# Optimization experiments

Hardware: AMD Instinct MI355X
Metric: run time of the kernel (lower is better)

Reference implementation:

```python
import jax, jax.numpy as jnp
import numpy as np

# ---- static configuration (matches init_kwargs) ----
B = 8; CIN = 3; COUT = 3
H_IN, W_IN = 128, 256          # img_size
H, W = 32, 64                  # internal grid = img_size / scale_factor
E = 256; HID = 512             # embed_dim, mlp hidden (ratio 2)
NR, NPHI = 3, 4                # DISCO kernel_shape
K = 1 + (NR - 1) * NPHI        # 9 piecewise-linear basis functions
LMAX = MMAX = H                # SHT truncation on internal grid
PI = np.pi

# ---- DISCO basis: psi[k, ho, hi, dlon] (quadrature folded in), stored as conj(rfft) over lon ----
def _build_psi(nlat_in, nlon_in, nlat_out, cutoff):
    ti = PI * (np.arange(nlat_in) + 0.5) / nlat_in
    to = PI * (np.arange(nlat_out) + 0.5) / nlat_out
    ph = 2 * PI * np.arange(nlon_in) / nlon_in
    cto, sto = np.cos(to)[:, None, None], np.sin(to)[:, None, None]
    cti, sti = np.cos(ti)[None, :, None], np.sin(ti)[None, :, None]
    cph, sph = np.cos(ph)[None, None, :], np.sin(ph)[None, None, :]
    r = np.arccos(np.clip(cto * cti + sto * sti * cph, -1.0, 1.0))      # great-circle dist
    alpha = np.arctan2(sti * sph, cti * sto - sti * cto * cph)          # azimuth
    dr = cutoff / (NR - 1); dphi = 2 * PI / NPHI
    quad = (sti * (PI / nlat_in) * (2 * PI / nlon_in)) * (r <= cutoff)  # quadrature * cutoff mask
    psi = np.empty((K, nlat_out, nlat_in, nlon_in), np.float32)
    psi[0] = np.clip(1 - r / dr, 0, 1) * quad                           # isotropic center basis
    for j in range(1, NR):
        tr = np.clip(1 - np.abs(r - j * dr) / dr, 0, 1)
        for k in range(NPHI):
            d = np.abs(np.mod(alpha - k * dphi + PI, 2 * PI) - PI)
            psi[1 + (j - 1) * NPHI + k] = tr * np.clip(1 - d / dphi, 0, 1) * quad
    return np.conj(np.fft.rfft(psi, axis=-1)).astype(np.complex64)

PSIH_ENC = jnp.asarray(_build_psi(H_IN, W_IN, H, 4 * PI / (H - 1)))
PSIH_INT = jnp.asarray(_build_psi(H, W, H, 4 * (NR + 1) * PI / (H - 1)))
PSIH_DEC = jnp.asarray(_build_psi(H_IN, W_IN, H_IN, 4 * PI / (H - 1)))

# ---- normalized associated Legendre for SHT on internal equiangular grid ----
def _legendre(lmax, theta):
    ct, st = np.cos(theta), np.sin(theta)
    P = np.zeros((lmax, lmax, theta.size))
    P[0, 0] = 1.0 / np.sqrt(2.0)
    for m in range(1, lmax):
        P[m, m] = np.sqrt((2 * m + 1) / (2.0 * m)) * st * P[m - 1, m - 1]
    for m in range(lmax - 1):
        P[m + 1, m] = np.sqrt(2 * m + 3.0) * ct * P[m, m]
    for m in range(lmax):
        for l in range(m + 2, lmax):
            a = np.sqrt((4.0 * l * l - 1) / (l * l - m * m))
            b = a * np.sqrt(((l - 1.0) ** 2 - m * m) / (4.0 * (l - 1) ** 2 - 1))
            P[l, m] = a * ct * P[l - 1, m] - b * P[l - 2, m]
    return P  # [l, m, h]

_THETA = PI * (np.arange(H) + 0.5) / H
_P = _legendre(LMAX, _THETA).astype(np.float32)
PW = jnp.asarray(_P * (np.sin(_THETA) * (PI / H))[None, None, :])  # analysis (with quadrature)
PT = jnp.asarray(_P)                                                # synthesis

# ---- bilinear resample (32,64)->(128,256), periodic in lon ----
_fi = np.clip((np.arange(H_IN) + 0.5) * H / H_IN - 0.5, 0, H - 1)
LAT_I0 = jnp.asarray(np.floor(_fi).astype(np.int32))
LAT_I1 = jnp.asarray(np.minimum(np.floor(_fi).astype(np.int32) + 1, H - 1))
LAT_W = jnp.asarray((_fi - np.floor(_fi)).astype(np.float32))
_fj = np.arange(W_IN) * W / W_IN
LON_J0 = jnp.asarray((np.floor(_fj).astype(np.int32)) % W)
LON_J1 = jnp.asarray((np.floor(_fj).astype(np.int32) + 1) % W)
LON_W = jnp.asarray((_fj - np.floor(_fj)).astype(np.float32))


def _disco(x, psih, n_in, stride):
    # circular cross-correlation over lon via FFT: z[b,c,k,ho,wo]
    Xh = jnp.fft.rfft(x, axis=-1)
    Zh = jnp.einsum('khim,bcim->bckhm', psih, Xh)
    return jnp.fft.irfft(Zh, n=n_in, axis=-1)[..., ::stride]


def _spectral(x, w):
    # driscoll-healy spectral conv: per-l channel mixing in SH space
    Xh = jnp.fft.rfft(x, axis=-1)[..., :MMAX]
    c = jnp.einsum('lmh,bchm->bclm', PW, Xh)
    c = jnp.einsum('ocl,bclm->bolm', w, c)
    Xo = jnp.einsum('lmh,bolm->bohm', PT, c)
    Xo = jnp.pad(Xo, ((0, 0), (0, 0), (0, 0), (0, W // 2 + 1 - MMAX)))
    return jnp.fft.irfft(Xo, n=W, axis=-1)


def _resample(x):
    a = jnp.take(x, LAT_I0, axis=2) * (1 - LAT_W)[:, None] + jnp.take(x, LAT_I1, axis=2) * LAT_W[:, None]
    return jnp.take(a, LON_J0, axis=3) * (1 - LON_W) + jnp.take(a, LON_J1, axis=3) * LON_W


def _forward(x, enc_w, lconv_w, gconv_w, mlp_w1, mlp_b1, mlp_w2, mlp_b2, skip_w, skip_b, dec_w):
    # encoder: DISCO conv (128,256)->(32,64), CIN->E
    z = _disco(x, PSIH_ENC, W_IN, W_IN // W)          # [B,CIN,K,32,64]
    x = jnp.einsum('ock,bckhw->bohw', enc_w, z)       # [B,E,32,64]
    for i in range(4):
        res = x
        if i % 2 == 0:  # local DISCO block
            z = _disco(x, PSIH_INT, W, 1)
            x = jnp.einsum('ock,bckhw->bohw', lconv_w[i // 2], z)
        else:           # global spectral (SHT) block
            x = _spectral(x, gconv_w[i // 2])
        # MLP (1x1 convs) + linear outer skip (norm = Identity)
        h = jax.nn.relu(jnp.einsum('oc,bchw->bohw', mlp_w1[i], x) + mlp_b1[i][:, None, None])
        x = jnp.einsum('oc,bchw->bohw', mlp_w2[i], h) + mlp_b2[i][:, None, None]
        x = x + jnp.einsum('oc,bchw->bohw', skip_w[i], res) + skip_b[i][:, None, None]
    # decoder: bilinear upsample then DISCO conv at full res, E->COUT (mix channels first: COUT small)
    x = _resample(x)                                  # [B,E,128,256]
    u = jnp.einsum('ock,bchw->bokhw', dec_w, x)       # [B,COUT,K,128,256]
    Uh = jnp.fft.rfft(u, axis=-1)
    Yh = jnp.einsum('khim,bokim->bohm', PSIH_DEC, Uh)
    return jnp.fft.irfft(Yh, n=W_IN, axis=-1)         # [B,COUT,128,256]


def setup_inputs() -> dict:
    key = jax.random.key(0)
    ks = jax.random.split(key, 8)
    f = jnp.float32
    return dict(
        x=jax.random.normal(ks[0], (B, CIN, H_IN, W_IN), f),
        enc_w=jax.random.normal(ks[1], (E, CIN, K), f) * float(1 / np.sqrt(CIN * K)),
        lconv_w=jax.random.normal(ks[2], (2, E, E, K), f) * float(1 / np.sqrt(E * K)),
        gconv_w=jax.random.normal(ks[3], (2, E, E, LMAX), f) * float(1 / np.sqrt(E)),
        mlp_w1=jax.random.normal(ks[4], (4, HID, E), f) * float(np.sqrt(2.0 / E)),
        mlp_b1=jnp.zeros((4, HID), f),
        mlp_w2=jax.random.normal(ks[5], (4, E, HID), f) * float(1 / np.sqrt(HID)),
        mlp_b2=jnp.zeros((4, E), f),
        skip_w=jax.random.normal(ks[6], (4, E, E), f) * float(np.sqrt(0.5 / E)),
        skip_b=jnp.zeros((4, E), f),
        dec_w=jax.random.normal(ks[7], (COUT, E, K), f) * float(1 / np.sqrt(E * K)),
    )


def reference(x, enc_w, lconv_w, gconv_w, mlp_w1, mlp_b1, mlp_w2, mlp_b2, skip_w, skip_b, dec_w):
    return _forward(x, enc_w, lconv_w, gconv_w, mlp_w1, mlp_b1, mlp_w2, mlp_b2, skip_w, skip_b, dec_w)
```

## Files before the change

kernel.cpp:

```cpp
#include <hip/hip_runtime.h>
#include <math.h>
#include <utility>

#define DI __device__ __forceinline__

namespace {

typedef unsigned short u16;
typedef unsigned int u32;
using f16x8 = __attribute__((ext_vector_type(8))) _Float16;
using f32x4 = __attribute__((ext_vector_type(4))) float;

constexpr int BB  = 8;
constexpr int CIN = 3;
constexpr int HIN = 128, WIN = 256;
constexpr int EE  = 256;
constexpr int NSP = BB * 32 * 64;
constexpr double PI_D = 3.14159265358979323846;
constexpr int ME_ENC = 5120, ME_INT = 2048, ME_DEC = 4608;
constexpr int HW_E = 34;

DI u16 f16rne(float x) { _Float16 h = (_Float16)x; return __builtin_bit_cast(unsigned short, h); }
DI float f16tof(u16 u) { return (float)__builtin_bit_cast(_Float16, u); }
DI u32 packhl(float v) {
  u16 h = f16rne(v);
  u16 l = f16rne(v - f16tof(h));
  return (u32)h | ((u32)l << 16);
}

DI bool psi_point(int nlat_in, int nlon_in, int nlat_out, double cutoff,
                  int ho, int hi, int d, bool wantv, float* out9)
{
  double ti = PI_D * (hi + 0.5) / nlat_in;
  double to = PI_D * (ho + 0.5) / nlat_out;
  double ph = 2.0 * PI_D * d / nlon_in;
  double cto = cos(to), sto = sin(to);
  double cti = cos(ti), sti = sin(ti);
  double cph = cos(ph), sph = sin(ph);
  double ca = cto * cti + sto * sti * cph;
  ca = fmin(1.0, fmax(-1.0, ca));
  double r = acos(ca);
  if (r > cutoff) return false;
  if (wantv) {
    double dr   = cutoff * 0.5;
    double dphi = PI_D * 0.5;
    double quad = sti * (PI_D / nlat_in) * (2.0 * PI_D / nlon_in);
    out9[0] = (float)(fmin(1.0, fmax(0.0, 1.0 - r / dr)) * quad);
    double alpha = atan2(sti * sph, cti * sto - sti * cto * cph);
#pragma unroll
    for (int j = 1; j <= 2; ++j) {
      double tr = fmin(1.0, fmax(0.0, 1.0 - fabs(r - j * dr) / dr));
#pragma unroll
      for (int k2 = 0; k2 < 4; ++k2) {
        double xx = alpha - k2 * dphi + PI_D;
        double yy = xx - 2.0 * PI_D * floor(xx / (2.0 * PI_D));
        double dd = fabs(yy - PI_D);
        out9[1 + (j - 1) * 4 + k2] = (float)(tr * fmin(1.0, fmax(0.0, 1.0 - dd / dphi)) * quad);
      }
    }
  }
  return true;
}

__global__ void k_psi_count(int nlat_in, int nlon_in, int nlat_out, double cutoff, int* cnt)
{
  int hi = blockIdx.x, ho = blockIdx.y, d = threadIdx.x;
  float dummy[9];
  bool in = psi_point(nlat_in, nlon_in, nlat_out, cutoff, ho, hi, d, false, dummy);
  unsigned long long mask = __ballot(in);
  if ((threadIdx.x & 63) == 0) {
    int tot = __popcll(mask);
    if (tot) atomicAdd(cnt + ho * nlat_in + hi, tot);
  }
}

__global__ void k_psi_scan(int nlat_in, int maxe, int* cnt, int* offs)
{
  int ho = blockIdx.x;
  int* c = cnt + ho * nlat_in;
  int* o = offs + ho * (nlat_in + 1);
  int run = 0;
  for (int hi = 0; hi < nlat_in; ++hi) {
    o[hi] = run < maxe ? run : maxe;
    run += c[hi];
    c[hi] = 0;
  }
  o[nlat_in] = run < maxe ? run : maxe;
}

__global__ void k_psi_fill(int nlat_in, int nlon_in, int nlat_out, double cutoff,
                           int maxe, int* cnt, const int* __restrict__ offs, float* __restrict__ tab)
{
  int hi = blockIdx.x, ho = blockIdx.y, d = threadIdx.x;
  float p9[9];
  bool in = psi_point(nlat_in, nlon_in, nlat_out, cutoff, ho, hi, d, true, p9);
  unsigned long long mask = __ballot(in);
  int lane = threadIdx.x & 63;
  int tot = __popcll(mask);
  int wbase = 0;
  if (lane == 0 && tot) wbase = atomicAdd(cnt + ho * nlat_in + hi, tot);
  wbase = __shfl(wbase, 0, 64);
  if (in) {
    int rank = __popcll(mask & ((1ull << lane) - 1ull));
    int idx = offs[ho * (nlat_in + 1) + hi] + wbase + rank;
    if (idx < maxe) {
      float* te = tab + ((size_t)ho * maxe + idx) * 12;
      te[0] = __int_as_float((hi << 16) | d);
#pragma unroll
      for (int k = 0; k < 9; ++k) te[1 + k] = p9[k];
      te[10] = 0.f; te[11] = 0.f;
    }
  }
}

__global__ void k_legendre(float* __restrict__ PW, float* __restrict__ PT)
{
  int h = threadIdx.x;
  if (h >= 32) return;
  double th = PI_D * (h + 0.5) / 32.0;
  double ct = cos(th), st = sin(th);
  double quad = st * (PI_D / 32.0);
  double diag = 0.70710678118654752440;
  for (int m = 0; m < 32; ++m) {
    if (m > 0) diag = sqrt((2.0 * m + 1.0) / (2.0 * m)) * st * diag;
    double plm2 = diag;
    PT[((size_t)m * 32 + m) * 32 + h] = (float)plm2;
    PW[((size_t)m * 32 + m) * 32 + h] = (float)(plm2 * quad);
    if (m + 1 < 32) {
      double plm1 = sqrt(2.0 * m + 3.0) * ct * diag;
      PT[((size_t)(m + 1) * 32 + m) * 32 + h] = (float)plm1;
      PW[((size_t)(m + 1) * 32 + m) * 32 + h] = (float)(plm1 * quad);
      for (int l = m + 2; l < 32; ++l) {
        double a  = sqrt((4.0 * l * l - 1.0) / ((double)l * l - (double)m * m));
        double bb = a * sqrt((((double)(l - 1) * (l - 1)) - (double)m * m) /
                             (4.0 * (double)(l - 1) * (l - 1) - 1.0));
        double p = a * ct * plm1 - bb * plm2;
        PT[((size_t)l * 32 + m) * 32 + h] = (float)p;
        PW[((size_t)l * 32 + m) * 32 + h] = (float)(p * quad);
        plm2 = plm1; plm1 = p;
      }
    }
    for (int l = 0; l < m; ++l) {
      PT[((size_t)l * 32 + m) * 32 + h] = 0.f;
      PW[((size_t)l * 32 + m) * 32 + h] = 0.f;
    }
  }
}

__global__ void k_tw(float* tc, float* ts)
{
  int t = blockIdx.x * 256 + threadIdx.x;
  if (t >= 33 * 64) return;
  int m = t >> 6, w = t & 63;
  double th = 2.0 * PI_D * m * w / 64.0;
  tc[t] = (float)cos(th);
  ts[t] = (float)sin(th);
}

__global__ void k_tw2(float* tc256, float* ts256, float* tc64, float* ts64)
{
  int t = threadIdx.x;
  double th = 2.0 * PI_D * t / 256.0;
  tc256[t] = (float)cos(th);
  ts256[t] = (float)sin(th);
  if (t < 64) {
    double th2 = 2.0 * PI_D * t / 64.0;
    tc64[t] = (float)cos(th2);
    ts64[t] = (float)sin(th2);
  }
}

__global__ void k_twmat(u32* __restrict__ tw256, u32* __restrict__ itw256,
                        u32* __restrict__ tw64, u32* __restrict__ itw64,
                        u32* __restrict__ iffold)
{
  int t = blockIdx.x * 256 + threadIdx.x;
  if (t < 256 * 129) {
    int w = t / 129, m = t % 129;
    double th = 2.0 * PI_D * ((m * w) & 255) / 256.0;
    tw256[w * 258 + 2 * m]     = packhl((float)cos(th));
    tw256[w * 258 + 2 * m + 1] = packhl((float)(-sin(th)));
  }
  if (t < 129 * 256) {
    int m = t >> 8, w = t & 255;
    double th = 2.0 * PI_D * ((m * w) & 255) / 256.0;
    float cr, ci;
    if (m == 0)        { cr = 1.f / 256.f; ci = 0.f; }
    else if (m == 128) { cr = ((w & 1) ? -1.f : 1.f) / 256.f; ci = 0.f; }
    else { cr = (float)(2.0 * cos(th) / 256.0); ci = (float)(-2.0 * sin(th) / 256.0); }
    itw256[(2 * m) * 256 + w] = packhl(cr);
    if (2 * m + 1 < 258) itw256[(2 * m + 1) * 256 + w] = packhl(ci);
  }
  if (t < 64 * 33) {
    int w = t / 33, m = t % 33;
    double th = 2.0 * PI_D * ((m * w) & 63) / 64.0;
    tw64[w * 66 + 2 * m]     = packhl((float)cos(th));
    tw64[w * 66 + 2 * m + 1] = packhl((float)(-sin(th)));
  }
  if (t < 33 * 64) {
    int m = t >> 6, w = t & 63;
    double th = 2.0 * PI_D * ((m * w) & 63) / 64.0;
    float cr, ci;
    if (m == 0)       { cr = 1.f / 64.f; ci = 0.f; }
    else if (m == 32) { cr = ((w & 1) ? -1.f : 1.f) / 64.f; ci = 0.f; }
    else { cr = (float)(2.0 * cos(th) / 64.0); ci = (float)(-2.0 * sin(th) / 64.0); }
    itw64[(2 * m) * 64 + w] = packhl(cr);
    if (2 * m + 1 < 66) itw64[(2 * m + 1) * 64 + w] = packhl(ci);
  }
  if (t < 129 * 64) {
    int m = t >> 6, wo = t & 63;
    double th = 2.0 * PI_D * ((m * wo) & 63) / 64.0;
    float cr, ci;
    if (m == 0)        { cr = 1.f / 256.f; ci = 0.f; }
    else if (m == 128) { cr = 1.f / 256.f; ci = 0.f; }
    else { cr = (float)(2.0 * cos(th) / 256.0); ci = (float)(-2.0 * sin(th) / 256.0); }
    iffold[(2 * m) * 64 + wo] = packhl(cr);
    if (2 * m + 1 < 258) iffold[(2 * m + 1) * 64 + wo] = packhl(ci);
  }
}

__global__ __launch_bounds__(256) void k_split(const float* __restrict__ in,
                                               u32* __restrict__ out, int n)
{
  for (int i = blockIdx.x * 256 + threadIdx.x; i < n; i += gridDim.x * 256)
    out[i] = packhl(in[i]);
}

__global__ void k_gwT_lp(const float* __restrict__ gw, u32* __restrict__ gwTlp)
{
  int idx = blockIdx.x * 256 + threadIdx.x;
  int c = idx & 255, o = (idx >> 8) & 255, l = idx >> 16;
  gwTlp[idx] = packhl(gw[((size_t)o * 256 + c) * 32 + l]);
}

__global__ void k_decT(const float* __restrict__ dw, float* __restrict__ dt)
{
  int idx = blockIdx.x * 256 + threadIdx.x;
  if (idx >= 27 * 256) return;
  int c = idx & 255, ok = idx >> 8;
  int o = ok / 9, k = ok % 9;
  dt[idx] = dw[((size_t)o * 256 + c) * 9 + k];
}

__global__ __launch_bounds__(320) void k_psih_dec(const int* __restrict__ off,
    const float* __restrict__ tab, const float* __restrict__ tc, const float* __restrict__ ts,
    float* __restrict__ psih)
{
  int ho = blockIdx.x, hw = blockIdx.y;
  int hi = ho - 16 + hw;
  int t = threadIdx.x;
  if (t >= 258) return;
  int m = t >> 1, ri = t & 1;
  const float* tw = ri ? ts : tc;
  float acc[9] = {};
  if (hi >= 0 && hi < 128) {
    int e0 = off[ho * 129 + hi], e1 = off[ho * 129 + hi + 1];
    const float* tb = tab + ((size_t)ho * ME_DEC + e0) * 12;
    for (int e = e0; e < e1; ++e, tb += 12) {
      int d = __float_as_int(tb[0]) & 0xffff;
      float v = tw[(m * d) & 255];
#pragma unroll
      for (int k = 0; k < 9; ++k) acc[k] += tb[1 + k] * v;
    }
  }
  size_t base = ((size_t)(ho * 33 + hw) * 9) * 258 + 2 * m + ri;
#pragma unroll
  for (int k = 0; k < 9; ++k) psih[base + (size_t)k * 258] = acc[k];
}

__global__ __launch_bounds__(128) void k_psih_int(const int* __restrict__ off,
    const float* __restrict__ tab, const float* __restrict__ tc, const float* __restrict__ ts,
    float* __restrict__ psih)
{
  int ho = blockIdx.x, hi = blockIdx.y;
  int t = threadIdx.x;
  if (t >= 66) return;
  int m = t >> 1, ri = t & 1;
  const float* tw = ri ? ts : tc;
  float acc[9] = {};
  int e0 = off[ho * 33 + hi], e1 = off[ho * 33 + hi + 1];
  const float* tb = tab + ((size_t)ho * ME_INT + e0) * 12;
  for (int e = e0; e < e1; ++e, tb += 12) {
    int d = __float_as_int(tb[0]) & 0xffff;
    float v = tw[(m * d) & 63];
#pragma unroll
    for (int k = 0; k < 9; ++k) acc[k] += tb[1 + k] * v;
  }
  size_t base = ((size_t)(ho * 32 + hi) * 9) * 66 + 2 * m + ri;
#pragma unroll
  for (int k = 0; k < 9; ++k) psih[base + (size_t)k * 66] = acc[k];
}

__global__ __launch_bounds__(320) void k_psih_enc(const int* __restrict__ off,
    const float* __restrict__ tab, const float* __restrict__ tc, const float* __restrict__ ts,
    float* __restrict__ psih)
{
  int ho = blockIdx.x, hw = blockIdx.y;
  int hi = 4 * ho - 15 + hw;
  int t = threadIdx.x;
  if (t >= 258) return;
  int m = t >> 1, ri = t & 1;
  const float* tw = ri ? ts : tc;
  float acc[9] = {};
  if (hi >= 0 && hi < 128) {
    int e0 = off[ho * 129 + hi], e1 = off[ho * 129 + hi + 1];
    const float* tb = tab + ((size_t)ho * ME_ENC + e0) * 12;
    for (int e = e0; e < e1; ++e, tb += 12) {
      int d = __float_as_int(tb[0]) & 0xffff;
      float v = tw[(m * d) & 255];
#pragma unroll
      for (int k = 0; k < 9; ++k) acc[k] += tb[1 + k] * v;
    }
  }
  size_t base = ((size_t)(ho * HW_E + hw) * 9) * 258 + 2 * m + ri;
#pragma unroll
  for (int k = 0; k < 9; ++k) psih[base + (size_t)k * 258] = acc[k];
}

__global__ __launch_bounds__(192) void k_enc_mconv(const float* __restrict__ psih,
    const float* __restrict__ XhE, float* __restrict__ Zh)
{
  int ho = blockIdx.x, cb = blockIdx.y;
  int c = cb >> 3, b = cb & 7;
  int m = threadIdx.x;
  if (m > 128) return;
  const float2* X2 = (const float2*)XhE;
  const float2* P2 = (const float2*)psih;
  float zr[9] = {}, zi[9] = {};
  int hi0 = 4 * ho - 15;
  for (int hw = 0; hw < HW_E; ++hw) {
    int hi = hi0 + hw;
    if (hi < 0 || hi > 127) continue;
    float2 xv = X2[((size_t)(b * 3 + c) * 128 + hi) * 129 + m];
    size_t pb = ((size_t)(ho * HW_E + hw) * 9) * 129 + m;
#pragma unroll
    for (int k = 0; k < 9; ++k) {
      float2 p = P2[pb + (size_t)k * 129];
      zr[k] += p.x * xv.x - p.y * xv.y;
      zi[k] += p.x * xv.y + p.y * xv.x;
    }
  }
#pragma unroll
  for (int k = 0; k < 9; ++k)
    ((float2*)Zh)[(((size_t)(c * 9 + k) * 8 + b) * 32 + ho) * 129 + m] =
        make_float2(zr[k], zi[k]);
}

__global__ __launch_bounds__(320) void k_int_mconv(const float* __restrict__ xh,
    const float* __restrict__ psih, float* __restrict__ zh, int c0)
{
  int ho = blockIdx.x, g = blockIdx.y, b = blockIdx.z;
  int t = threadIdx.x;
  if (t >= 264) return;
  int cl = t / 33, m = t % 33;
  int c = c0 + g * 8 + cl;
  const float2* X2 = (const float2*)xh;
  const float2* P2 = (const float2*)psih;
  float zr[9] = {}, zi[9] = {};
  for (int hi = 0; hi < 32; ++hi) {
    float2 xv = X2[((size_t)(c * 8 + b) * 32 + hi) * 33 + m];
    size_t pb = ((size_t)(ho * 32 + hi) * 9) * 33 + m;
#pragma unroll
    for (int k = 0; k < 9; ++k) {
      float2 p = P2[pb + (size_t)k * 33];
      zr[k] += p.x * xv.x - p.y * xv.y;
      zi[k] += p.x * xv.y + p.y * xv.x;
    }
  }
  int crow = (g * 8 + cl) * 9;
#pragma unroll
  for (int k = 0; k < 9; ++k)
    ((float2*)zh)[((size_t)(crow + k)) * 8448 + b * 1056 + ho * 33 + m] =
        make_float2(zr[k], zi[k]);
}

__global__ __launch_bounds__(192) void k_dec_mconv(const float* __restrict__ psih,
    const float* __restrict__ gh, float* __restrict__ yh)
{
  int ho = blockIdx.x, b = blockIdx.y;
  int m = threadIdx.x;
  if (m > 128) return;
  const float2* P2 = (const float2*)psih;
  const float2* G2 = (const float2*)gh;
  float yr[3] = {}, yi[3] = {};
  for (int hw = 0; hw < 33; ++hw) {
    int hi = ho - 16 + hw;
    if (hi < 0 || hi > 127) continue;
    size_t pb = ((size_t)(ho * 33 + hw) * 9) * 129 + m;
#pragma unroll
    for (int k = 0; k < 9; ++k) {
      float2 p = P2[pb + (size_t)k * 129];
#pragma unroll
      for (int o = 0; o < 3; ++o) {
        float2 gv = G2[((size_t)((o * 9 + k) * 8 + b) * 128 + hi) * 129 + m];
        yr[o] += p.x * gv.x - p.y * gv.y;
        yi[o] += p.x * gv.y + p.y * gv.x;
      }
    }
  }
#pragma unroll
  for (int o = 0; o < 3; ++o)
    ((float2*)yh)[((size_t)(b * 3 + o) * 128 + ho) * 129 + m] = make_float2(yr[o], yi[o]);
}

__global__ __launch_bounds__(256) void k_gemm(
    int M, int N, int K,
    const float* __restrict__ A, const u32* __restrict__ Ap, int lda, long long sA,
    const float* __restrict__ Bm, const u32* __restrict__ Bp, int ldb, long long sB,
    float* __restrict__ C, int ldc, long long sC,
    const float* __restrict__ bias, int flags)
{
  if (A)  A  += (size_t)blockIdx.z * sA;
  if (Ap) Ap += (size_t)blockIdx.z * sA;
  if (Bm) Bm += (size_t)blockIdx.z * sB;
  if (Bp) Bp += (size_t)blockIdx.z * sB;
  C += (size_t)blockIdx.z * sC;
  __shared__ alignas(16) u16 Ah[128 * 40], Al[128 * 40], Bh[128 * 40], Bl[128 * 40];
  int bm = blockIdx.y * 128, bn = blockIdx.x * 128;
  int tid = threadIdx.x;
  int sr = tid >> 1, k2 = tid & 1;
  int lane = tid & 63, wid = tid >> 6;
  int wr = wid >> 1, wc = wid & 1;
  int lrow = lane & 15, kg = lane >> 4;
  f32x4 acc[4][4] = {};
  bool bok = (bn + sr) < N;

  for (int k0 = 0; k0 < K; k0 += 32) {
    {
      u32* ph = (u32*)&Ah[sr * 40 + k2 * 16];
      u32* pl = (u32*)&Al[sr * 40 + k2 * 16];
      if (Ap) {
        const u32* Ar = Ap + (size_t)(bm + sr) * lda + k0 + k2 * 16;
#pragma unroll
        for (int j2 = 0; j2 < 8; ++j2) {
          int gk = k0 + k2 * 16 + 2 * j2;
          u32 w0 = (gk < K)     ? Ar[2 * j2]     : 0u;
          u32 w1 = (gk + 1 < K) ? Ar[2 * j2 + 1] : 0u;
          ph[j2] = (w0 & 0xffffu) | (w1 << 16);
          pl[j2] = (w0 >> 16) | (w1 & 0xffff0000u);
        }
      } else {
        const float* Ar = A + (size_t)(bm + sr) * lda + k0 + k2 * 16;
#pragma unroll
        for (int j2 = 0; j2 < 8; ++j2) {
          int gk = k0 + k2 * 16 + 2 * j2;
          float v0 = (gk < K)     ? Ar[2 * j2]     : 0.f;
          float v1 = (gk + 1 < K) ? Ar[2 * j2 + 1] : 0.f;
          u16 h0 = f16rne(v0), h1 = f16rne(v1);
          u16 l0 = f16rne(v0 - f16tof(h0)), l1 = f16rne(v1 - f16tof(h1));
          ph[j2] = (u32)h0 | ((u32)h1 << 16);
          pl[j2] = (u32)l0 | ((u32)l1 << 16);
        }
      }
    }
    {
      u32* ph = (u32*)&Bh[sr * 40 + k2 * 16];
      u32* pl = (u32*)&Bl[sr * 40 + k2 * 16];
      if (Bp) {
        const u32* Bc = Bp + bn + sr;
#pragma unroll
        for (int j2 = 0; j2 < 8; ++j2) {
          int gk = k0 + k2 * 16 + 2 * j2;
          u32 w0 = (bok && gk < K)     ? Bc[(size_t)gk * ldb]       : 0u;
          u32 w1 = (bok && gk + 1 < K) ? Bc[(size_t)(gk + 1) * ldb] : 0u;
          ph[j2] = (w0 & 0xffffu) | (w1 << 16);
          pl[j2] = (w0 >> 16) | (w1 & 0xffff0000u);
        }
      } else {
        const float* Bc = Bm + bn + sr;
#pragma unroll
        for (int j2 = 0; j2 < 8; ++j2) {
          int gk = k0 + k2 * 16 + 2 * j2;
          float v0 = (bok && gk < K)     ? Bc[(size_t)gk * ldb]       : 0.f;
          float v1 = (bok && gk + 1 < K) ? Bc[(size_t)(gk + 1) * ldb] : 0.f;
          u16 h0 = f16rne(v0), h1 = f16rne(v1);
          u16 l0 = f16rne(v0 - f16tof(h0)), l1 = f16rne(v1 - f16tof(h1));
          ph[j2] = (u32)h0 | ((u32)h1 << 16);
          pl[j2] = (u32)l0 | ((u32)l1 << 16);
        }
      }
    }
    __syncthreads();
    f16x8 fah[4], fal[4], fbh[4], fbl[4];
#pragma unroll
    for (int i = 0; i < 4; ++i) {
      int ar = wr * 64 + i * 16 + lrow;
      fah[i] = *(const f16x8*)&Ah[ar * 40 + kg * 8];
      fal[i] = *(const f16x8*)&Al[ar * 40 + kg * 8];
      int br = wc * 64 + i * 16 + lrow;
      fbh[i] = *(const f16x8*)&Bh[br * 40 + kg * 8];
      fbl[i] = *(const f16x8*)&Bl[br * 40 + kg * 8];
    }
#pragma unroll
    for (int i = 0; i < 4; ++i)
#pragma unroll
      for (int j = 0; j < 4; ++j) {
        acc[i][j] = __builtin_amdgcn_mfma_f32_16x16x32_f16(fah[i], fbh[j], acc[i][j], 0, 0, 0);
        acc[i][j] = __builtin_amdgcn_mfma_f32_16x16x32_f16(fah[i], fbl[j], acc[i][j], 0, 0, 0);
        acc[i][j] = __builtin_amdgcn_mfma_f32_16x16x32_f16(fal[i], fbh[j], acc[i][j], 0, 0, 0);
      }
    __syncthreads();
  }

#pragma unroll
  for (int i = 0; i < 4; ++i) {
    int gm0 = bm + wr * 64 + i * 16 + kg * 4;
#pragma unroll
    for (int j = 0; j < 4; ++j) {
      int gn = bn + wc * 64 + j * 16 + lrow;
      if (gn >= N) continue;
#pragma unroll
      for (int rr = 0; rr < 4; ++rr) {
        int gm = gm0 + rr;
        size_t idx = (size_t)gm * ldc + gn;
        float v = acc[i][j][rr];
        if (flags & 4) v += bias[gm];
        if (flags & 2) v += C[idx];
        if (flags & 1) v = fmaxf(v, 0.f);
        C[idx] = v;
      }
    }
  }
}

__global__ __launch_bounds__(256) void k_gemm_m27(const float* __restrict__ A,
    const float* __restrict__ Bm, float* __restrict__ C)
{
  int n = blockIdx.x * 256 + threadIdx.x;
  float acc[27] = {};
  for (int k = 0; k < 256; ++k) {
    float bv = Bm[(size_t)k * NSP + n];
#pragma unroll
    for (int m = 0; m < 27; ++m) acc[m] += A[m * 256 + k] * bv;
  }
#pragma unroll
  for (int m = 0; m < 27; ++m) C[(size_t)m * NSP + n] = acc[m];
}

__global__ __launch_bounds__(64) void k_analysis(const float* __restrict__ PW,
    const float* __restrict__ Xh, float* __restrict__ c1)
{
  int l = blockIdx.x, c = blockIdx.y, b = blockIdx.z;
  int t = threadIdx.x, m = t >> 1, ri = t & 1;
  const float* xr = Xh + ((size_t)(c * 8 + b) * 32) * 66;
  const float* pw = PW + ((size_t)l * 32 + m) * 32;
  float acc = 0.f;
  for (int h = 0; h < 32; ++h) acc += pw[h] * xr[h * 66 + 2 * m + ri];
  c1[(((size_t)l * EE + c) * 8 + b) * 64 + 2 * m + ri] = acc;
}

__global__ __launch_bounds__(64) void k_synth(const float* __restrict__ PT,
    const float* __restrict__ c2, const float* __restrict__ tc, const float* __restrict__ ts,
    float* __restrict__ outact)
{
  int h = blockIdx.x, o = blockIdx.y, b = blockIdx.z;
  int t = threadIdx.x;
  __shared__ float Xo[64];
  {
    int m = t >> 1, ri = t & 1;
    float acc = 0.f;
    for (int l = m; l < 32; ++l)
      acc += PT[((size_t)l * 32 + m) * 32 + h] *
             c2[(((size_t)l * EE + o) * 8 + b) * 64 + 2 * m + ri];
    Xo[t] = acc;
  }
  __syncthreads();
  float y = Xo[0];
  for (int m = 1; m < 32; ++m)
    y += 2.f * (Xo[2 * m] * tc[m * 64 + t] - Xo[2 * m + 1] * ts[m * 64 + t]);
  outact[(size_t)o * NSP + b * 2048 + h * 64 + t] = y * (1.f / 64.f);
}

__global__ __launch_bounds__(256) void k_resample(const float* __restrict__ gi, float* __restrict__ gf)
{
  int t = blockIdx.x * 256 + threadIdx.x;
  int WO = t & 255, HO = (t >> 8) & 127, b = (t >> 15) & 7, ok = t >> 18;
  float fi = fminf(fmaxf(HO * 0.25f - 0.375f, 0.f), 31.f);
  int i0 = (int)fi;
  int i1 = min(i0 + 1, 31);
  float wi = fi - (float)i0;
  int j0 = WO >> 2;
  int j1 = (j0 + 1) & 63;
  float wj = (float)(WO & 3) * 0.25f;
  const float* s = gi + (size_t)ok * NSP + b * 2048;
  float v00 = s[i0 * 64 + j0], v01 = s[i0 * 64 + j1];
  float v10 = s[i1 * 64 + j0], v11 = s[i1 * 64 + j1];
  float a0 = v00 * (1.f - wj) + v01 * wj;
  float a1 = v10 * (1.f - wj) + v11 * wj;
  gf[((size_t)ok * 8 + b) * 32768 + HO * 256 + WO] = a0 * (1.f - wi) + a1 * wi;
}

}

extern "C" void kernel_launch(void* const* d_in, const int* in_sizes, int n_in,
                              void* d_out, int out_size, void* d_ws, size_t ws_size,
                              hipStream_t stream)
{
  const float* x_in  = (const float*)d_in[0];
  const float* enc_w = (const float*)d_in[1];
  const float* lconv = (const float*)d_in[2];
  const float* gconv = (const float*)d_in[3];
  const float* w1    = (const float*)d_in[4];
  const float* b1    = (const float*)d_in[5];
  const float* w2    = (const float*)d_in[6];
  const float* b2    = (const float*)d_in[7];
  const float* skw   = (const float*)d_in[8];
  const float* skb   = (const float*)d_in[9];
  const float* decw  = (const float*)d_in[10];
  float* out = (float*)d_out;

  char* ws = (char*)d_ws;
  size_t off = 0;
  auto alloc = [&](size_t nfloats) -> float* {
    float* p = (float*)(ws + off);
    off += ((nfloats * 4 + 255) / 256) * 256;
    return p;
  };
  float* PW    = alloc(32768);
  float* PT    = alloc(32768);
  float* tcos  = alloc(33 * 64);
  float* tsin  = alloc(33 * 64);
  float* tc256 = alloc(256);
  float* ts256 = alloc(256);
  float* tc64  = alloc(64);
  float* ts64  = alloc(64);
  u32* TW256p  = (u32*)alloc(256 * 258);
  u32* ITW256p = (u32*)alloc(258 * 256);
  u32* TW64p   = (u32*)alloc(64 * 66);
  u32* ITW64p  = (u32*)alloc(66 * 64);
  u32* IFp     = (u32*)alloc(258 * 64);
  int*   cnt2  = (int*)alloc(21504);
  int*   cnt_enc = cnt2;
  int*   cnt_int = cnt2 + 4096;
  int*   cnt_dec = cnt2 + 5120;
  int*   off_enc = (int*)alloc(32 * 129);
  int*   off_int = (int*)alloc(32 * 33);
  int*   off_dec = (int*)alloc(128 * 129);
  float* decT     = alloc(27 * 256);
  float* psih_dec = alloc((size_t)128 * 33 * 9 * 258);
  float* psih_int = alloc((size_t)32 * 32 * 9 * 66);
  float* psih_enc = alloc((size_t)32 * HW_E * 9 * 258);
  u32* enc_wp = (u32*)alloc(256 * 27);
  u32* w1p    = (u32*)alloc(4 * 512 * 256);
  u32* w2p    = (u32*)alloc(4 * 256 * 512);
  u32* skwp   = (u32*)alloc(4 * 256 * 256);
  u32* lconvp = (u32*)alloc(2 * 256 * 2304);
  float* P  = alloc((size_t)EE * NSP);
  float* Q  = alloc((size_t)EE * NSP);
  float* T  = alloc((size_t)EE * NSP);
  float* U  = alloc(18382848);
  (void)ws_size; (void)in_sizes; (void)n_in; (void)out_size;

  float* tab_dec = U;
  float* tab_int = U + 7077888;
  float* tab_enc = U + 7864320;
  float* zc      = U;
  float* XhE     = U + 442368;
  float* ZhE     = U + 1234944;
  float* XH      = U;
  float* ZH      = U + 4325376;
  float* XO      = U + 14057472;
  float* c1s     = U + 4325376;
  float* c2s     = U + 8519680;
  u32*   gwTlp   = (u32*)(U + 12713984);
  float* Hb      = U;
  u32*   DYNp    = (u32*)(U + 8388608);
  float* g_int   = U;
  float* g_full  = U + 524288;
  float* GH      = U + 7602176;
  float* YH      = U + 14735360;

  const double CUT_LOC = 4.0 * PI_D / 31.0;
  const double CUT_INT = 16.0 * PI_D / 31.0;
  auto splitN = [&](const float* src, u32* dst, int n) {
    int g = (n + 255) / 256; if (g > 2048) g = 2048;
    hipLaunchKernelGGL(k_split, dim3(g), dim3(256), 0, stream, src, dst, n);
  };

  hipMemsetAsync(cnt2, 0, 21504 * 4, stream);
  hipLaunchKernelGGL(k_legendre, dim3(1), dim3(64), 0, stream, PW, PT);
  hipLaunchKernelGGL(k_tw,  dim3(9), dim3(256), 0, stream, tcos, tsin);
  hipLaunchKernelGGL(k_tw2, dim3(1), dim3(256), 0, stream, tc256, ts256, tc64, ts64);
  hipLaunchKernelGGL(k_twmat, dim3(129), dim3(256), 0, stream, TW256p, ITW256p, TW64p, ITW64p, IFp);
  hipLaunchKernelGGL(k_decT, dim3(27), dim3(256), 0, stream, decw, decT);
  splitN(enc_w, enc_wp, 256 * 27);
  splitN(w1,    w1p,    4 * 512 * 256);
  splitN(w2,    w2p,    4 * 256 * 512);
  splitN(skw,   skwp,   4 * 256 * 256);
  splitN(lconv, lconvp, 2 * 256 * 2304);

  hipLaunchKernelGGL(k_psi_count, dim3(128, 32), dim3(256), 0, stream, 128, 256, 32, CUT_LOC, cnt_enc);
  hipLaunchKernelGGL(k_psi_scan,  dim3(32), dim3(1), 0, stream, 128, ME_ENC, cnt_enc, off_enc);
  hipLaunchKernelGGL(k_psi_fill,  dim3(128, 32), dim3(256), 0, stream, 128, 256, 32, CUT_LOC, ME_ENC, cnt_enc, off_enc, tab_enc);

  hipLaunchKernelGGL(k_psi_count, dim3(32, 32), dim3(64), 0, stream, 32, 64, 32, CUT_INT, cnt_int);
  hipLaunchKernelGGL(k_psi_scan,  dim3(32), dim3(1), 0, stream, 32, ME_INT, cnt_int, off_int);
  hipLaunchKernelGGL(k_psi_fill,  dim3(32, 32), dim3(64), 0, stream, 32, 64, 32, CUT_INT, ME_INT, cnt_int, off_int, tab_int);

  hipLaunchKernelGGL(k_psi_count, dim3(128, 128), dim3(256), 0, stream, 128, 256, 128, CUT_LOC, cnt_dec);
  hipLaunchKernelGGL(k_psi_scan,  dim3(128), dim3(1), 0, stream, 128, ME_DEC, cnt_dec, off_dec);
  hipLaunchKernelGGL(k_psi_fill,  dim3(128, 128), dim3(256), 0, stream, 128, 256, 128, CUT_LOC, ME_DEC, cnt_dec, off_dec, tab_dec);

  hipLaunchKernelGGL(k_psih_dec, dim3(128, 33), dim3(320), 0, stream, off_dec, tab_dec, tc256, ts256, psih_dec);
  hipLaunchKernelGGL(k_psih_int, dim3(32, 32),  dim3(128), 0, stream, off_int, tab_int, tc64, ts64, psih_int);
  hipLaunchKernelGGL(k_psih_enc, dim3(32, HW_E), dim3(320), 0, stream, off_enc, tab_enc, tc256, ts256, psih_enc);

  hipLaunchKernelGGL(k_gemm, dim3(3, 24, 1), dim3(256), 0, stream,
                     3072, 258, 256, x_in, (const u32*)nullptr, 256, 0LL,
                     (const float*)nullptr, TW256p, 258, 0LL,
                     XhE, 258, 0LL, (const float*)nullptr, 0);
  hipLaunchKernelGGL(k_enc_mconv, dim3(32, 24), dim3(192), 0, stream, psih_enc, XhE, ZhE);
  hipLaunchKernelGGL(k_gemm, dim3(1, 54, 1), dim3(256), 0, stream,
                     6912, 64, 258, ZhE, (const u32*)nullptr, 258, 0LL,
                     (const float*)nullptr, IFp, 64, 0LL,
                     zc, 64, 0LL, (const float*)nullptr, 0);
  hipLaunchKernelGGL(k_gemm, dim3(128, 2, 1), dim3(256), 0, stream,
                     256, NSP, 27, (const float*)nullptr, enc_wp, 27, 0LL,
                     zc, (const u32*)nullptr, NSP, 0LL,
                     P, NSP, 0LL, (const float*)nullptr, 0);

  for (int i = 0; i < 4; ++i) {
    int layer = i >> 1;
    if ((i & 1) == 0) {
      hipLaunchKernelGGL(k_gemm, dim3(1, 512, 1), dim3(256), 0, stream,
                         65536, 66, 64, P, (const u32*)nullptr, 64, 0LL,
                         (const float*)nullptr, TW64p, 66, 0LL,
                         XH, 66, 0LL, (const float*)nullptr, 0);
      for (int cc = 0; cc < 4; ++cc) {
        hipLaunchKernelGGL(k_int_mconv, dim3(32, 8, 8), dim3(320), 0, stream,
                           XH, psih_int, ZH, cc * 64);
        hipLaunchKernelGGL(k_gemm, dim3(132, 2, 1), dim3(256), 0, stream,
                           256, 16896, 576,
                           (const float*)nullptr, lconvp + (size_t)layer * 589824 + cc * 576, 2304, 0LL,
                           ZH, (const u32*)nullptr, 16896, 0LL,
                           XO, 16896, 0LL, (const float*)nullptr, cc ? 2 : 0);
      }
      hipLaunchKernelGGL(k_gemm, dim3(1, 512, 1), dim3(256), 0, stream,
                         65536, 64, 66, XO, (const u32*)nullptr, 66, 0LL,
                         (const float*)nullptr, ITW64p, 64, 0LL,
                         T, 64, 0LL, (const float*)nullptr, 0);
    } else {
      hipLaunchKernelGGL(k_gwT_lp, dim3(8192), dim3(256), 0, stream,
                         gconv + (size_t)layer * 2097152, gwTlp);
      hipLaunchKernelGGL(k_gemm, dim3(1, 512, 1), dim3(256), 0, stream,
                         65536, 66, 64, P, (const u32*)nullptr, 64, 0LL,
                         (const float*)nullptr, TW64p, 66, 0LL,
                         XH, 66, 0LL, (const float*)nullptr, 0);
      hipLaunchKernelGGL(k_analysis, dim3(32, 256, 8), dim3(64), 0, stream, PW, XH, c1s);
      hipLaunchKernelGGL(k_gemm, dim3(4, 2, 32), dim3(256), 0, stream,
                         256, 512, 256,
                         (const float*)nullptr, gwTlp, 256, 65536LL,
                         c1s, (const u32*)nullptr, 512, 131072LL,
                         c2s, 512, 131072LL, (const float*)nullptr, 0);
      hipLaunchKernelGGL(k_synth, dim3(32, 256, 8), dim3(64), 0, stream, PT, c2s, tcos, tsin, T);
    }
    splitN(T, DYNp, EE * NSP);
    hipLaunchKernelGGL(k_gemm, dim3(128, 4, 1), dim3(256), 0, stream,
                       512, NSP, 256, (const float*)nullptr, w1p + (size_t)i * 131072, 256, 0LL,
                       (const float*)nullptr, DYNp, NSP, 0LL,
                       Hb, NSP, 0LL, b1 + (size_t)i * 512, 5);
    splitN(Hb, DYNp, 512 * NSP);
    hipLaunchKernelGGL(k_gemm, dim3(128, 2, 1), dim3(256), 0, stream,
                       256, NSP, 512, (const float*)nullptr, w2p + (size_t)i * 131072, 512, 0LL,
                       (const float*)nullptr, DYNp, NSP, 0LL,
                       Q, NSP, 0LL, b2 + (size_t)i * 256, 4);
    splitN(P, DYNp, EE * NSP);
    hipLaunchKernelGGL(k_gemm, dim3(128, 2, 1), dim3(256), 0, stream,
                       256, NSP, 256, (const float*)nullptr, skwp + (size_t)i * 65536, 256, 0LL,
                       (const float*)nullptr, DYNp, NSP, 0LL,
                       Q, NSP, 0LL, skb + (size_t)i * 256, 6);
    std::swap(P, Q);
  }

  hipLaunchKernelGGL(k_gemm_m27, dim3(64), dim3(256), 0, stream, decT, P, g_int);
  hipLaunchKernelGGL(k_resample, dim3(27648), dim3(256), 0, stream, g_int, g_full);
  hipLaunchKernelGGL(k_gemm, dim3(3, 216, 1), dim3(256), 0, stream,
                     27648, 258, 256, g_full, (const u32*)nullptr, 256, 0LL,
                     (const float*)nullptr, TW256p, 258, 0LL,
                     GH, 258, 0LL, (const float*)nullptr, 0);
  hipLaunchKernelGGL(k_dec_mconv, dim3(128, 8), dim3(192), 0, stream, psih_dec, GH, YH);
  hipLaunchKernelGGL(k_gemm, dim3(2, 24, 1), dim3(256), 0, stream,
                     3072, 256, 258, YH, (const u32*)nullptr, 258, 0LL,
                     (const float*)nullptr, ITW256p, 256, 0LL,
                     out, 256, 0LL, (const float*)nullptr, 0);
}
```

Measured before the change: 5.215 ms.

## Fold SHT into dense GEMMs and emit packed split-fp16 from GEMM epilogues

Replaces the scalar analysis and synthesis kernels of the spherical convolution with two 2048x2048 GEMMs. Their precomputed matrices fold the Legendre weights and the longitude DFT twiddles together, and transpose kernels sit between them and the per-l channel GEMM. The GEMM epilogue gains a flag that writes the hi/lo fp16 split form directly, so the separate split passes over T and the MLP hidden buffer go away. The LDS row stride also changes from 40 to 36. The dense GEMMs do more raw FLOPs than the triangular Legendre sums and need 32 MB of extra matrices, which trades arithmetic for matrix-core use.

```diff
diff --git a/kernel.cpp b/kernel.cpp
--- a/kernel.cpp
+++ b/kernel.cpp
@@ -147,16 +147,6 @@
   }
 }
 
-__global__ void k_tw(float* tc, float* ts)
-{
-  int t = blockIdx.x * 256 + threadIdx.x;
-  if (t >= 33 * 64) return;
-  int m = t >> 6, w = t & 63;
-  double th = 2.0 * PI_D * m * w / 64.0;
-  tc[t] = (float)cos(th);
-  ts[t] = (float)sin(th);
-}
-
 __global__ void k_tw2(float* tc256, float* ts256, float* tc64, float* ts64)
 {
   int t = threadIdx.x;
@@ -219,11 +209,50 @@
   }
 }
 
+__global__ __launch_bounds__(256) void k_m1m2(const float* __restrict__ PW, const float* __restrict__ PT,
+    const float* __restrict__ tc64, const float* __restrict__ ts64,
+    u32* __restrict__ M1p, u32* __restrict__ M2p)
+{
+  int t = blockIdx.x * 256 + threadIdx.x;
+  int cidx = t & 2047, ridx = t >> 11;
+  {
+    int l = cidx >> 6, q = cidx & 63, m = q >> 1, ri = q & 1;
+    int h = ridx >> 6, w = ridx & 63;
+    float tw = ri ? -ts64[(m * w) & 63] : tc64[(m * w) & 63];
+    M1p[(size_t)ridx * 2048 + cidx] = packhl(PW[((size_t)l * 32 + m) * 32 + h] * tw);
+  }
+  {
+    int l = ridx >> 6, q = ridx & 63, m = q >> 1, ri = q & 1;
+    int h = cidx >> 6, w = cidx & 63;
+    float coef = PT[((size_t)l * 32 + m) * 32 + h];
+    float v;
+    if (m == 0) v = ri ? 0.f : coef * (1.f / 64.f);
+    else {
+      float tw = ri ? -ts64[(m * w) & 63] : tc64[(m * w) & 63];
+      v = coef * tw * (2.f / 64.f);
+    }
+    M2p[(size_t)ridx * 2048 + cidx] = packhl(v);
+  }
+}
+
 __global__ __launch_bounds__(256) void k_split(const float* __restrict__ in,
                                                u32* __restrict__ out, int n)
 {
   for (int i = blockIdx.x * 256 + threadIdx.x; i < n; i += gridDim.x * 256)
     out[i] = packhl(in[i]);
+}
+
+__global__ __launch_bounds__(256) void k_t1(const float* __restrict__ src, u32* __restrict__ dst)
+{
+  int t = blockIdx.x * 256 + threadIdx.x;
+  int q = t & 63, b = (t >> 6) & 7, c = (t >> 9) & 255, l = t >> 17;
+  dst[t] = packhl(src[((size_t)(c * 8 + b)) * 2048 + l * 64 + q]);
+}
+__global__ __launch_bounds__(256) void k_t2(const float* __restrict__ src, u32* __restrict__ dst)
+{
+  int t = blockIdx.x * 256 + threadIdx.x;
+  int q = t & 63, l = (t >> 6) & 31, b = (t >> 11) & 7, o = t >> 14;
+  dst[t] = packhl(src[((size_t)(l * 256 + o)) * 512 + b * 64 + q]);
 }
 
 __global__ void k_gwT_lp(const float* __restrict__ gw, u32* __restrict__ gwTlp)
@@ -407,15 +436,16 @@
     int M, int N, int K,
     const float* __restrict__ A, const u32* __restrict__ Ap, int lda, long long sA,
     const float* __restrict__ Bm, const u32* __restrict__ Bp, int ldb, long long sB,
-    float* __restrict__ C, int ldc, long long sC,
+    float* __restrict__ C, int ldc, long long sC, u32* __restrict__ Cp,
     const float* __restrict__ bias, int flags)
 {
   if (A)  A  += (size_t)blockIdx.z * sA;
   if (Ap) Ap += (size_t)blockIdx.z * sA;
   if (Bm) Bm += (size_t)blockIdx.z * sB;
   if (Bp) Bp += (size_t)blockIdx.z * sB;
-  C += (size_t)blockIdx.z * sC;
-  __shared__ alignas(16) u16 Ah[128 * 40], Al[128 * 40], Bh[128 * 40], Bl[128 * 40];
+  if (C)  C  += (size_t)blockIdx.z * sC;
+  if (Cp) Cp += (size_t)blockIdx.z * sC;
+  __shared__ alignas(16) u16 Ah[128 * 36], Al[128 * 36], Bh[128 * 36], Bl[128 * 36];
   int bm = blockIdx.y * 128, bn = blockIdx.x * 128;
   int tid = threadIdx.x;
   int sr = tid >> 1, k2 = tid & 1;
@@ -427,8 +457,8 @@
 
   for (int k0 = 0; k0 < K; k0 += 32) {
     {
-      u32* ph = (u32*)&Ah[sr * 40 + k2 * 16];
-      u32* pl = (u32*)&Al[sr * 40 + k2 * 16];
+      u32* ph = (u32*)&Ah[sr * 36 + k2 * 16];
+      u32* pl = (u32*)&Al[sr * 36 + k2 * 16];
       if (Ap) {
         const u32* Ar = Ap + (size_t)(bm + sr) * lda + k0 + k2 * 16;
 #pragma unroll
@@ -454,8 +484,8 @@
       }
     }
     {
-      u32* ph = (u32*)&Bh[sr * 40 + k2 * 16];
-      u32* pl = (u32*)&Bl[sr * 40 + k2 * 16];
+      u32* ph = (u32*)&Bh[sr * 36 + k2 * 16];
+      u32* pl = (u32*)&Bl[sr * 36 + k2 * 16];
       if (Bp) {
         const u32* Bc = Bp + bn + sr;
 #pragma unroll
@@ -485,11 +515,11 @@
 #pragma unroll
     for (int i = 0; i < 4; ++i) {
       int ar = wr * 64 + i * 16 + lrow;
-      fah[i] = *(const f16x8*)&Ah[ar * 40 + kg * 8];
-      fal[i] = *(const f16x8*)&Al[ar * 40 + kg * 8];
+      fah[i] = *(const f16x8*)&Ah[ar * 36 + kg * 8];
+      fal[i] = *(const f16x8*)&Al[ar * 36 + kg * 8];
       int br = wc * 64 + i * 16 + lrow;
-      fbh[i] = *(const f16x8*)&Bh[br * 40 + kg * 8];
-      fbl[i] = *(const f16x8*)&Bl[br * 40 + kg * 8];
+      fbh[i] = *(const f16x8*)&Bh[br * 36 + kg * 8];
+      fbl[i] = *(const f16x8*)&Bl[br * 36 + kg * 8];
     }
 #pragma unroll
     for (int i = 0; i < 4; ++i)
@@ -517,7 +547,8 @@
         if (flags & 4) v += bias[gm];
         if (flags & 2) v += C[idx];
         if (flags & 1) v = fmaxf(v, 0.f);
-        C[idx] = v;
+        if (C) C[idx] = v;
+        if (flags & 8) Cp[idx] = packhl(v);
       }
     }
   }
@@ -535,40 +566,6 @@
   }
 #pragma unroll
   for (int m = 0; m < 27; ++m) C[(size_t)m * NSP + n] = acc[m];
-}
-
-__global__ __launch_bounds__(64) void k_analysis(const float* __restrict__ PW,
-    const float* __restrict__ Xh, float* __restrict__ c1)
-{
-  int l = blockIdx.x, c = blockIdx.y, b = blockIdx.z;
-  int t = threadIdx.x, m = t >> 1, ri = t & 1;
-  const float* xr = Xh + ((size_t)(c * 8 + b) * 32) * 66;
-  const float* pw = PW + ((size_t)l * 32 + m) * 32;
-  float acc = 0.f;
-  for (int h = 0; h < 32; ++h) acc += pw[h] * xr[h * 66 + 2 * m + ri];
-  c1[(((size_t)l * EE + c) * 8 + b) * 64 + 2 * m + ri] = acc;
-}
-
-__global__ __launch_bounds__(64) void k_synth(const float* __restrict__ PT,
-    const float* __restrict__ c2, const float* __restrict__ tc, const float* __restrict__ ts,
-    float* __restrict__ outact)
-{
-  int h = blockIdx.x, o = blockIdx.y, b = blockIdx.z;
-  int t = threadIdx.x;
-  __shared__ float Xo[64];
-  {
-    int m = t >> 1, ri = t & 1;
-    float acc = 0.f;
-    for (int l = m; l < 32; ++l)
-      acc += PT[((size_t)l * 32 + m) * 32 + h] *
-             c2[(((size_t)l * EE + o) * 8 + b) * 64 + 2 * m + ri];
-    Xo[t] = acc;
-  }
-  __syncthreads();
-  float y = Xo[0];
-  for (int m = 1; m < 32; ++m)
-    y += 2.f * (Xo[2 * m] * tc[m * 64 + t] - Xo[2 * m + 1] * ts[m * 64 + t]);
-  outact[(size_t)o * NSP + b * 2048 + h * 64 + t] = y * (1.f / 64.f);
 }
 
 __global__ __launch_bounds__(256) void k_resample(const float* __restrict__ gi, float* __restrict__ gf)
@@ -618,8 +615,6 @@
   };
   float* PW    = alloc(32768);
   float* PT    = alloc(32768);
-  float* tcos  = alloc(33 * 64);
-  float* tsin  = alloc(33 * 64);
   float* tc256 = alloc(256);
   float* ts256 = alloc(256);
   float* tc64  = alloc(64);
@@ -629,6 +624,8 @@
   u32* TW64p   = (u32*)alloc(64 * 66);
   u32* ITW64p  = (u32*)alloc(66 * 64);
   u32* IFp     = (u32*)alloc(258 * 64);
+  u32* M1p     = (u32*)alloc((size_t)2048 * 2048);
+  u32* M2p     = (u32*)alloc((size_t)2048 * 2048);
   int*   cnt2  = (int*)alloc(21504);
   int*   cnt_enc = cnt2;
   int*   cnt_int = cnt2 + 4096;
@@ -648,7 +645,8 @@
   float* P  = alloc((size_t)EE * NSP);
   float* Q  = alloc((size_t)EE * NSP);
   float* T  = alloc((size_t)EE * NSP);
-  float* U  = alloc(18382848);
+  u32*   Tp = (u32*)alloc((size_t)EE * NSP);
+  float* U  = alloc(18874368);
   (void)ws_size; (void)in_sizes; (void)n_in; (void)out_size;
 
   float* tab_dec = U;
@@ -660,11 +658,13 @@
   float* XH      = U;
   float* ZH      = U + 4325376;
   float* XO      = U + 14057472;
-  float* c1s     = U + 4325376;
-  float* c2s     = U + 8519680;
-  u32*   gwTlp   = (u32*)(U + 12713984);
-  float* Hb      = U;
-  u32*   DYNp    = (u32*)(U + 8388608);
+  u32*   gwTlp   = (u32*)U;
+  float* c1cb    = U + 2097152;
+  u32*   c1sp    = (u32*)(U + 6291456);
+  float* c2s     = U + 10485760;
+  u32*   c2tp    = (u32*)(U + 14680064);
+  u32*   Hbp     = (u32*)U;
+  u32*   Pp      = (u32*)(U + 8388608);
   float* g_int   = U;
   float* g_full  = U + 524288;
   float* GH      = U + 7602176;
@@ -676,12 +676,13 @@
     int g = (n + 255) / 256; if (g > 2048) g = 2048;
     hipLaunchKernelGGL(k_split, dim3(g), dim3(256), 0, stream, src, dst, n);
   };
+  const float* F0 = nullptr; const u32* U0 = nullptr; u32* W0 = nullptr;
 
   hipMemsetAsync(cnt2, 0, 21504 * 4, stream);
   hipLaunchKernelGGL(k_legendre, dim3(1), dim3(64), 0, stream, PW, PT);
-  hipLaunchKernelGGL(k_tw,  dim3(9), dim3(256), 0, stream, tcos, tsin);
   hipLaunchKernelGGL(k_tw2, dim3(1), dim3(256), 0, stream, tc256, ts256, tc64, ts64);
   hipLaunchKernelGGL(k_twmat, dim3(129), dim3(256), 0, stream, TW256p, ITW256p, TW64p, ITW64p, IFp);
+  hipLaunchKernelGGL(k_m1m2, dim3(16384), dim3(256), 0, stream, PW, PT, tc64, ts64, M1p, M2p);
   hipLaunchKernelGGL(k_decT, dim3(27), dim3(256), 0, stream, decw, decT);
   splitN(enc_w, enc_wp, 256 * 27);
   splitN(w1,    w1p,    4 * 512 * 256);
@@ -706,81 +707,73 @@
   hipLaunchKernelGGL(k_psih_enc, dim3(32, HW_E), dim3(320), 0, stream, off_enc, tab_enc, tc256, ts256, psih_enc);
 
   hipLaunchKernelGGL(k_gemm, dim3(3, 24, 1), dim3(256), 0, stream,
-                     3072, 258, 256, x_in, (const u32*)nullptr, 256, 0LL,
-                     (const float*)nullptr, TW256p, 258, 0LL,
-                     XhE, 258, 0LL, (const float*)nullptr, 0);
+                     3072, 258, 256, x_in, U0, 256, 0LL, F0, TW256p, 258, 0LL,
+                     XhE, 258, 0LL, W0, F0, 0);
   hipLaunchKernelGGL(k_enc_mconv, dim3(32, 24), dim3(192), 0, stream, psih_enc, XhE, ZhE);
   hipLaunchKernelGGL(k_gemm, dim3(1, 54, 1), dim3(256), 0, stream,
-                     6912, 64, 258, ZhE, (const u32*)nullptr, 258, 0LL,
-                     (const float*)nullptr, IFp, 64, 0LL,
-                     zc, 64, 0LL, (const float*)nullptr, 0);
+                     6912, 64, 258, ZhE, U0, 258, 0LL, F0, IFp, 64, 0LL,
+                     zc, 64, 0LL, W0, F0, 0);
   hipLaunchKernelGGL(k_gemm, dim3(128, 2, 1), dim3(256), 0, stream,
-                     256, NSP, 27, (const float*)nullptr, enc_wp, 27, 0LL,
-                     zc, (const u32*)nullptr, NSP, 0LL,
-                     P, NSP, 0LL, (const float*)nullptr, 0);
+                     256, NSP, 27, F0, enc_wp, 27, 0LL, zc, U0, NSP, 0LL,
+                     P, NSP, 0LL, W0, F0, 0);
 
   for (int i = 0; i < 4; ++i) {
     int layer = i >> 1;
     if ((i & 1) == 0) {
       hipLaunchKernelGGL(k_gemm, dim3(1, 512, 1), dim3(256), 0, stream,
-                         65536, 66, 64, P, (const u32*)nullptr, 64, 0LL,
-                         (const float*)nullptr, TW64p, 66, 0LL,
-                         XH, 66, 0LL, (const float*)nullptr, 0);
+                         65536, 66, 64, P, U0, 64, 0LL, F0, TW64p, 66, 0LL,
+                         XH, 66, 0LL, W0, F0, 0);
       for (int cc = 0; cc < 4; ++cc) {
         hipLaunchKernelGGL(k_int_mconv, dim3(32, 8, 8), dim3(320), 0, stream,
                            XH, psih_int, ZH, cc * 64);
         hipLaunchKernelGGL(k_gemm, dim3(132, 2, 1), dim3(256), 0, stream,
                            256, 16896, 576,
-                           (const float*)nullptr, lconvp + (size_t)layer * 589824 + cc * 576, 2304, 0LL,
-                           ZH, (const u32*)nullptr, 16896, 0LL,
-                           XO, 16896, 0LL, (const float*)nullptr, cc ? 2 : 0);
+                           F0, lconvp + (size_t)layer * 589824 + cc * 576, 2304, 0LL,
+                           ZH, U0, 16896, 0LL,
+                           XO, 16896, 0LL, W0, F0, cc ? 2 : 0);
       }
       hipLaunchKernelGGL(k_gemm, dim3(1, 512, 1), dim3(256), 0, stream,
-                         65536, 64, 66, XO, (const u32*)nullptr, 66, 0LL,
-                         (const float*)nullptr, ITW64p, 64, 0LL,
-                         T, 64, 0LL, (const float*)nullptr, 0);
+                         65536, 64, 66, XO, U0, 66, 0LL, F0, ITW64p, 64, 0LL,
+                         T, 64, 0LL, Tp, F0, 8);
     } else {
       hipLaunchKernelGGL(k_gwT_lp, dim3(8192), dim3(256), 0, stream,
                          gconv + (size_t)layer * 2097152, gwTlp);
-      hipLaunchKernelGGL(k_gemm, dim3(1, 512, 1), dim3(256), 0, stream,
-                         65536, 66, 64, P, (const u32*)nullptr, 64, 0LL,
-                         (const float*)nullptr, TW64p, 66, 0LL,
-                         XH, 66, 0LL, (const float*)nullptr, 0);
-      hipLaunchKernelGGL(k_analysis, dim3(32, 256, 8), dim3(64), 0, stream, PW, XH, c1s);
+      hipLaunchKernelGGL(k_gemm, dim3(16, 16, 1), dim3(256), 0, stream,
+                         2048, 2048, 2048, P, U0, 2048, 0LL, F0, M1p, 2048, 0LL,
+                         c1cb, 2048, 0LL, W0, F0, 0);
+      hipLaunchKernelGGL(k_t1, dim3(16384), dim3(256), 0, stream, c1cb, c1sp);
       hipLaunchKernelGGL(k_gemm, dim3(4, 2, 32), dim3(256), 0, stream,
                          256, 512, 256,
-                         (const float*)nullptr, gwTlp, 256, 65536LL,
-                         c1s, (const u32*)nullptr, 512, 131072LL,
-                         c2s, 512, 131072LL, (const float*)nullptr, 0);
-      hipLaunchKernelGGL(k_synth, dim3(32, 256, 8), dim3(64), 0, stream, PT, c2s, tcos, tsin, T);
-    }
-    splitN(T, DYNp, EE * NSP);
+                         F0, gwTlp, 256, 65536LL, F0, c1sp, 512, 131072LL,
+                         c2s, 512, 131072LL, W0, F0, 0);
+      hipLaunchKernelGGL(k_t2, dim3(16384), dim3(256), 0, stream, c2s, c2tp);
+      hipLaunchKernelGGL(k_gemm, dim3(16, 16, 1), dim3(256), 0, stream,
+                         2048, 2048, 2048, F0, c2tp, 2048, 0LL, F0, M2p, 2048, 0LL,
+                         T, 2048, 0LL, Tp, F0, 8);
+    }
     hipLaunchKernelGGL(k_gemm, dim3(128, 4, 1), dim3(256), 0, stream,
-                       512, NSP, 256, (const float*)nullptr, w1p + (size_t)i * 131072, 256, 0LL,
-                       (const float*)nullptr, DYNp, NSP, 0LL,
-                       Hb, NSP, 0LL, b1 + (size_t)i * 512, 5);
-    splitN(Hb, DYNp, 512 * NSP);
+                       512, NSP, 256, F0, w1p + (size_t)i * 131072, 256, 0LL,
+                       F0, Tp, NSP, 0LL,
+                       (float*)nullptr, NSP, 0LL, Hbp, b1 + (size_t)i * 512, 1 | 4 | 8);
     hipLaunchKernelGGL(k_gemm, dim3(128, 2, 1), dim3(256), 0, stream,
-                       256, NSP, 512, (const float*)nullptr, w2p + (size_t)i * 131072, 512, 0LL,
-                       (const float*)nullptr, DYNp, NSP, 0LL,
-                       Q, NSP, 0LL, b2 + (size_t)i * 256, 4);
-    splitN(P, DYNp, EE * NSP);
+                       256, NSP, 512, F0, w2p + (size_t)i * 131072, 512, 0LL,
+                       F0, Hbp, NSP, 0LL,
+                       Q, NSP, 0LL, W0, b2 + (size_t)i * 256, 4);
+    splitN(P, Pp, EE * NSP);
     hipLaunchKernelGGL(k_gemm, dim3(128, 2, 1), dim3(256), 0, stream,
-                       256, NSP, 256, (const float*)nullptr, skwp + (size_t)i * 65536, 256, 0LL,
-                       (const float*)nullptr, DYNp, NSP, 0LL,
-                       Q, NSP, 0LL, skb + (size_t)i * 256, 6);
+                       256, NSP, 256, F0, skwp + (size_t)i * 65536, 256, 0LL,
+                       F0, Pp, NSP, 0LL,
+                       Q, NSP, 0LL, W0, skb + (size_t)i * 256, 2 | 4);
     std::swap(P, Q);
   }
 
   hipLaunchKernelGGL(k_gemm_m27, dim3(64), dim3(256), 0, stream, decT, P, g_int);
   hipLaunchKernelGGL(k_resample, dim3(27648), dim3(256), 0, stream, g_int, g_full);
   hipLaunchKernelGGL(k_gemm, dim3(3, 216, 1), dim3(256), 0, stream,
-                     27648, 258, 256, g_full, (const u32*)nullptr, 256, 0LL,
-                     (const float*)nullptr, TW256p, 258, 0LL,
-                     GH, 258, 0LL, (const float*)nullptr, 0);
+                     27648, 258, 256, g_full, U0, 256, 0LL, F0, TW256p, 258, 0LL,
+                     GH, 258, 0LL, W0, F0, 0);
   hipLaunchKernelGGL(k_dec_mconv, dim3(128, 8), dim3(192), 0, stream, psih_dec, GH, YH);
   hipLaunchKernelGGL(k_gemm, dim3(2, 24, 1), dim3(256), 0, stream,
-                     3072, 256, 258, YH, (const u32*)nullptr, 258, 0LL,
-                     (const float*)nullptr, ITW256p, 256, 0LL,
-                     out, 256, 0LL, (const float*)nullptr, 0);
-}
+                     3072, 256, 258, YH, U0, 258, 0LL, F0, ITW256p, 256, 0LL,
+                     out, 256, 0LL, W0, F0, 0);
+}
```

New measurement: 5.919 ms. +13.5%, slower.
